# Kernel optimization log

Measured on AMD Instinct MI355X. Metric: run time of the kernel, lower is better.

## Reference

```python
import jax, jax.numpy as jnp
import numpy as np

N_NODES = 100000
N_EDGES = 3200000
D_IN, D_HID, D_OUT = 256, 256, 256
B, V, C = 64, 50, 64
DEC_H1, DEC_H2, N_CLS = 512, 256, 1000
NEG_INF = -1e9


def setup_inputs() -> dict:
    key = jax.random.key(0)
    ks = jax.random.split(key, 20)
    s = lambda d: 1.0 / np.sqrt(d)
    return {
        'edge_index': jax.random.randint(ks[0], (2, N_EDGES), 0, N_NODES, dtype=jnp.int64 if jax.config.jax_enable_x64 else jnp.int32),
        'edge_weight': jax.random.uniform(ks[1], (N_EDGES,), dtype=jnp.float32),
        'codes_x': jax.random.randint(ks[2], (B, V, C), 0, N_NODES, dtype=jnp.int64 if jax.config.jax_enable_x64 else jnp.int32),
        'node_emb': jax.random.normal(ks[3], (N_NODES, D_IN), jnp.float32) * 0.02,
        'W1': jax.random.normal(ks[4], (D_IN, D_HID), jnp.float32) * s(D_IN),
        'b1': jnp.zeros((D_HID,), jnp.float32),
        'W2': jax.random.normal(ks[5], (D_HID, D_OUT), jnp.float32) * s(D_HID),
        'b2': jnp.zeros((D_OUT,), jnp.float32),
        'Wv': jax.random.normal(ks[6], (D_OUT, D_OUT), jnp.float32) * s(D_OUT),
        'uv': jax.random.normal(ks[7], (D_OUT,), jnp.float32) * s(D_OUT),
        'Wp': jax.random.normal(ks[8], (D_OUT, D_OUT), jnp.float32) * s(D_OUT),
        'up': jax.random.normal(ks[9], (D_OUT,), jnp.float32) * s(D_OUT),
        'Wd1': jax.random.normal(ks[10], (D_OUT, DEC_H1), jnp.float32) * s(D_OUT),
        'bd1': jnp.zeros((DEC_H1,), jnp.float32),
        'Wd2': jax.random.normal(ks[11], (DEC_H1, DEC_H2), jnp.float32) * s(DEC_H1),
        'bd2': jnp.zeros((DEC_H2,), jnp.float32),
        'Wd3': jax.random.normal(ks[12], (DEC_H2, N_CLS), jnp.float32) * s(DEC_H2),
        'bd3': jnp.zeros((N_CLS,), jnp.float32),
    }


def reference(edge_index, edge_weight, codes_x, node_emb, W1, b1, W2, b2,
              Wv, uv, Wp, up, Wd1, bd1, Wd2, bd2, Wd3, bd3):
    n = node_emb.shape[0]
    src, dst = edge_index[0], edge_index[1]

    def agg(x):  # weighted message passing: out_i = sum_{e: dst=i} w_e * x[src_e]
        return jax.ops.segment_sum(x[src] * edge_weight[:, None], dst, num_segments=n)

    # 2-layer weighted GCN over the code ontology graph (dropout in eval mode)
    h = jax.nn.relu(agg(node_emb) @ W1 + b1)          # [N, D_hid]
    emb = agg(h) @ W2 + b2                             # [N, D_out]

    # Ragged per-visit code attention, vectorized with masks (code id 0 = padding)
    code_mask = codes_x > 0                            # [B, V, C]
    ce = emb[codes_x]                                  # [B, V, C, D]
    ev = jnp.tanh(jnp.einsum('bvcd,de->bvce', ce, Wv)) @ uv   # [B, V, C]
    av = jax.nn.softmax(jnp.where(code_mask, ev, NEG_INF), axis=-1)
    vemb = jnp.einsum('bvc,bvcd->bvd', av, ce)         # [B, V, D]
    visit_mask = code_mask.any(-1)                     # [B, V]
    vemb = jnp.where(visit_mask[..., None], vemb, 0.0)

    # Per-patient visit attention over valid visits only
    ep = jnp.tanh(vemb @ Wp) @ up                      # [B, V]
    ap = jax.nn.softmax(jnp.where(visit_mask, ep, NEG_INF), axis=-1)
    pemb = jnp.einsum('bv,bvd->bd', ap, vemb)          # [B, D]
    pemb = jnp.where(visit_mask.any(-1)[:, None], pemb, 0.0)  # empty patient -> zeros

    # Decoder MLP classifier (train_type='direct')
    h1 = jax.nn.relu(pemb @ Wd1 + bd1)
    h2 = jax.nn.relu(h1 @ Wd2 + bd2)
    return h2 @ Wd3 + bd3                              # [B, n_classes]
```

## Files before the change

kernel.cpp:

```cpp
#include <hip/hip_runtime.h>
#include <hip/hip_bf16.h>
#include <math.h>


#define D 256
#define BPAT 64
#define VIS 50
#define CODES 64
#define NEG_INF -1e9f
#define MPAD 100096
#define BINB 32
#define NBIN 3125
#define SORTCAP 1536

typedef unsigned short ushort_t;
typedef short short8 __attribute__((ext_vector_type(8)));
typedef float f32x4 __attribute__((ext_vector_type(4)));

__device__ __forceinline__ float blo(unsigned u) { return __uint_as_float(u << 16); }
__device__ __forceinline__ float bhi(unsigned u) { return __uint_as_float(u & 0xffff0000u); }
__device__ __forceinline__ float bf2f(ushort_t u) { return __uint_as_float((unsigned)u << 16); }
__device__ __forceinline__ ushort_t f2bfu(float f) {
    __hip_bfloat16 h = __float2bfloat16(f);
    return *reinterpret_cast<ushort_t*>(&h);
}
__device__ __forceinline__ unsigned pack2(float a, float b) {
    return (unsigned)f2bfu(a) | ((unsigned)f2bfu(b) << 16);
}


__global__ __launch_bounds__(512) void bin_count_kernel(
    const int* __restrict__ ei, int* __restrict__ bincount, int ne) {
    __shared__ int h[NBIN];
    for (int i = threadIdx.x; i < NBIN; i += 512) h[i] = 0;
    __syncthreads();
    int stride = gridDim.x * 512;
    for (int e = blockIdx.x * 512 + threadIdx.x; e < ne; e += stride)
        atomicAdd(&h[ei[(size_t)ne + e] >> 5], 1);
    __syncthreads();
    for (int i = threadIdx.x; i < NBIN; i += 512) {
        int c = h[i];
        if (c) atomicAdd(&bincount[i], c);
    }
}

__global__ __launch_bounds__(64) void bin_scan_kernel(
    const int* __restrict__ bincount, int* __restrict__ binstart,
    int* __restrict__ bincursor, int* __restrict__ rp, int ne, int nn) {
    __shared__ int carry;
    int lane = threadIdx.x;
    if (lane == 0) carry = 0;
    __syncthreads();
    for (int base = 0; base < NBIN; base += 64) {
        int i = base + lane;
        int v = (i < NBIN) ? bincount[i] : 0;
        int x = v;
        #pragma unroll
        for (int d = 1; d < 64; d <<= 1) {
            int y = __shfl_up(x, (unsigned)d, 64);
            if (lane >= d) x += y;
        }
        int c = carry;
        if (i < NBIN) { int ex = c + x - v; binstart[i] = ex; bincursor[i] = ex; }
        __syncthreads();
        if (lane == 63) carry = c + x;
        __syncthreads();
    }
    if (lane == 0) { binstart[NBIN] = ne; rp[nn] = ne; }
}

__global__ __launch_bounds__(512) void partition_kernel(
    const int* __restrict__ ei, const float* __restrict__ ew,
    int* __restrict__ bincursor, uint2* __restrict__ ptmp, int ne) {
    __shared__ int h[NBIN];
    __shared__ int base_[NBIN];
    for (int i = threadIdx.x; i < NBIN; i += 512) h[i] = 0;
    __syncthreads();
    int stride = gridDim.x * 512;
    for (int e = blockIdx.x * 512 + threadIdx.x; e < ne; e += stride)
        atomicAdd(&h[ei[(size_t)ne + e] >> 5], 1);
    __syncthreads();
    for (int i = threadIdx.x; i < NBIN; i += 512) {
        int c = h[i];
        base_[i] = c ? atomicAdd(&bincursor[i], c) : 0;
        h[i] = 0;
    }
    __syncthreads();
    for (int e = blockIdx.x * 512 + threadIdx.x; e < ne; e += stride) {
        int dd = ei[(size_t)ne + e];
        int ss = ei[e];
        float w = ew[e];
        int bin = dd >> 5;
        int r = atomicAdd(&h[bin], 1);
        ptmp[base_[bin] + r] =
            make_uint2((unsigned)ss | ((unsigned)(dd & 31) << 17),
                       __float_as_uint(w));
    }
}

__global__ __launch_bounds__(256) void binsort_kernel(
    const uint2* __restrict__ ptmp, const int* __restrict__ binstart,
    uint2* __restrict__ epair, int* __restrict__ rp) {
    int b = blockIdx.x;
    int tid = threadIdx.x;
    int beg = binstart[b], end = binstart[b + 1];
    int nE = end - beg;
    __shared__ uint2 sbuf[SORTCAP];
    __shared__ int cnt[BINB];
    __shared__ int cur[BINB];
    if (tid < BINB) cnt[tid] = 0;
    __syncthreads();
    if (nE <= SORTCAP) {
        for (int i = tid; i < nE; i += 256) {
            uint2 p = ptmp[beg + i];
            sbuf[i] = p;
            atomicAdd(&cnt[(p.x >> 17) & 31], 1);
        }
        __syncthreads();
        if (tid < BINB) {
            int v = cnt[tid];
            int x = v;
            #pragma unroll
            for (int d = 1; d < BINB; d <<= 1) {
                int y = __shfl_up(x, (unsigned)d, BINB);
                if (tid >= d) x += y;
            }
            int start = beg + x - v;
            cur[tid] = start;
            rp[b * BINB + tid] = start;
        }
        __syncthreads();
        for (int i = tid; i < nE; i += 256) {
            uint2 p = sbuf[i];
            int dl = (p.x >> 17) & 31;
            int pos = atomicAdd(&cur[dl], 1);
            epair[pos] = make_uint2(p.x & 0x1FFFF, p.y);
        }
    } else {
        for (int i = beg + tid; i < end; i += 256)
            atomicAdd(&cnt[(ptmp[i].x >> 17) & 31], 1);
        __syncthreads();
        if (tid < BINB) {
            int v = cnt[tid];
            int x = v;
            #pragma unroll
            for (int d = 1; d < BINB; d <<= 1) {
                int y = __shfl_up(x, (unsigned)d, BINB);
                if (tid >= d) x += y;
            }
            int start = beg + x - v;
            cur[tid] = start;
            rp[b * BINB + tid] = start;
        }
        __syncthreads();
        for (int i = beg + tid; i < end; i += 256) {
            uint2 p = ptmp[i];
            int dl = (p.x >> 17) & 31;
            int pos = atomicAdd(&cur[dl], 1);
            epair[pos] = make_uint2(p.x & 0x1FFFF, p.y);
        }
    }
}

__global__ void cvt_node_kernel(const float* __restrict__ in, ushort_t* __restrict__ out,
                                long n_valid, long n_total) {
    long g = (long)blockIdx.x * blockDim.x + threadIdx.x;
    long ng = n_total >> 2;
    for (long i = g; i < ng; i += (long)gridDim.x * blockDim.x) {
        long e = i << 2;
        uint2 o;
        if (e < n_valid) {
            float4 v = ((const float4*)in)[i];
            o.x = pack2(v.x, v.y);
            o.y = pack2(v.z, v.w);
        } else {
            o.x = 0u; o.y = 0u;
        }
        ((uint2*)out)[i] = o;
    }
}

__global__ __launch_bounds__(256) void transpose_w4_kernel(
    const float* __restrict__ Wa, const float* __restrict__ Wb,
    const float* __restrict__ Wc, const float* __restrict__ Wd,
    ushort_t* __restrict__ Ta, ushort_t* __restrict__ Tb,
    ushort_t* __restrict__ Tc, ushort_t* __restrict__ Td) {
    const float* W;
    ushort_t* Wt;
    switch (blockIdx.z) {
        case 0: W = Wa; Wt = Ta; break;
        case 1: W = Wb; Wt = Tb; break;
        case 2: W = Wc; Wt = Tc; break;
        default: W = Wd; Wt = Td; break;
    }
    __shared__ float t[32][33];
    int bx = blockIdx.x * 32;
    int by = blockIdx.y * 32;
    int lx = threadIdx.x & 31, ly = threadIdx.x >> 5;
    #pragma unroll
    for (int i = 0; i < 32; i += 8)
        t[ly + i][lx] = W[(size_t)(by + ly + i) * 256 + bx + lx];
    __syncthreads();
    #pragma unroll
    for (int i = 0; i < 32; i += 8)
        Wt[(size_t)(bx + ly + i) * 256 + by + lx] = f2bfu(t[lx][ly + i]);
}

__device__ __forceinline__ void acc8(float* a, uint4 v, float w) {
    a[0] += w * blo(v.x); a[1] += w * bhi(v.x);
    a[2] += w * blo(v.y); a[3] += w * bhi(v.y);
    a[4] += w * blo(v.z); a[5] += w * bhi(v.z);
    a[6] += w * blo(v.w); a[7] += w * bhi(v.w);
}

__global__ __launch_bounds__(256) void agg_bf16_kernel(
    const ushort_t* __restrict__ x, const int* __restrict__ rp,
    const uint2* __restrict__ ep, ushort_t* __restrict__ out, int n) {
    int wv = (int)(((size_t)blockIdx.x * blockDim.x + threadIdx.x) >> 6);
    int lane = threadIdx.x & 63;
    if (wv >= n) return;
    int half = lane >> 5;
    int l32 = lane & 31;
    int beg = rp[wv], end = rp[wv + 1];
    float a[8] = {};
    int e = beg;
    for (; e + 16 <= end; e += 16) {
        uint2 p0 = ep[e + half];
        uint2 p1 = ep[e + 2 + half];
        uint2 p2 = ep[e + 4 + half];
        uint2 p3 = ep[e + 6 + half];
        uint2 p4 = ep[e + 8 + half];
        uint2 p5 = ep[e + 10 + half];
        uint2 p6 = ep[e + 12 + half];
        uint2 p7 = ep[e + 14 + half];
        uint4 v0 = ((const uint4*)(x + (size_t)p0.x * D))[l32];
        uint4 v1 = ((const uint4*)(x + (size_t)p1.x * D))[l32];
        uint4 v2 = ((const uint4*)(x + (size_t)p2.x * D))[l32];
        uint4 v3 = ((const uint4*)(x + (size_t)p3.x * D))[l32];
        uint4 v4 = ((const uint4*)(x + (size_t)p4.x * D))[l32];
        uint4 v5 = ((const uint4*)(x + (size_t)p5.x * D))[l32];
        uint4 v6 = ((const uint4*)(x + (size_t)p6.x * D))[l32];
        uint4 v7 = ((const uint4*)(x + (size_t)p7.x * D))[l32];
        acc8(a, v0, __uint_as_float(p0.y));
        acc8(a, v1, __uint_as_float(p1.y));
        acc8(a, v2, __uint_as_float(p2.y));
        acc8(a, v3, __uint_as_float(p3.y));
        acc8(a, v4, __uint_as_float(p4.y));
        acc8(a, v5, __uint_as_float(p5.y));
        acc8(a, v6, __uint_as_float(p6.y));
        acc8(a, v7, __uint_as_float(p7.y));
    }
    for (; e + 4 <= end; e += 4) {
        uint2 p0 = ep[e + half];
        uint2 p1 = ep[e + 2 + half];
        uint4 v0 = ((const uint4*)(x + (size_t)p0.x * D))[l32];
        uint4 v1 = ((const uint4*)(x + (size_t)p1.x * D))[l32];
        acc8(a, v0, __uint_as_float(p0.y));
        acc8(a, v1, __uint_as_float(p1.y));
    }
    for (; e + 2 <= end; e += 2) {
        uint2 p0 = ep[e + half];
        uint4 v0 = ((const uint4*)(x + (size_t)p0.x * D))[l32];
        acc8(a, v0, __uint_as_float(p0.y));
    }
    if (e < end) {
        uint2 p0 = ep[e];
        uint4 v0 = ((const uint4*)(x + (size_t)p0.x * D))[l32];
        acc8(a, v0, half ? 0.f : __uint_as_float(p0.y));
    }
    #pragma unroll
    for (int j = 0; j < 8; ++j) a[j] += __shfl_xor(a[j], 32, 64);
    if (half == 0) {
        uint4 o;
        o.x = pack2(a[0], a[1]); o.y = pack2(a[2], a[3]);
        o.z = pack2(a[4], a[5]); o.w = pack2(a[6], a[7]);
        ((uint4*)(out + (size_t)wv * D))[l32] = o;
    }
}

template<int MODE>
__global__ __launch_bounds__(512) void mfma_gemm_kernel(
    const ushort_t* __restrict__ A, const ushort_t* __restrict__ Wt,
    const float* __restrict__ bias, ushort_t* __restrict__ out,
    const float* __restrict__ u, float* __restrict__ tout, int mvalid) {
    __shared__ __align__(16) ushort_t As[128 * 32];
    __shared__ __align__(16) ushort_t Bs[256 * 32];
    __shared__ float s_t[128];
    const int tid = threadIdx.x;
    const int lane = tid & 63;
    const int wv = tid >> 6;
    const int wr = wv >> 2, wc = wv & 3;
    const size_t brow = (size_t)blockIdx.x * 128;

    const int ra = tid >> 2, ca = tid & 3;
    const int rb1 = ra + 128;
    const int csa = ca ^ ((ra >> 1) & 3);
    const ushort_t* gA  = A  + (brow + ra) * 256 + ca * 8;
    const ushort_t* gB0 = Wt + (size_t)ra  * 256 + ca * 8;
    const ushort_t* gB1 = Wt + (size_t)rb1 * 256 + ca * 8;
    ushort_t* lA  = As + ra * 32 + csa * 8;
    ushort_t* lB0 = Bs + ra * 32 + csa * 8;
    ushort_t* lB1 = Bs + rb1 * 32 + csa * 8;

    const int g = lane >> 4, rl = lane & 15;
    int aoff[4], boff[4];
    #pragma unroll
    for (int m = 0; m < 4; ++m) {
        int row = wr * 64 + m * 16 + rl;
        aoff[m] = row * 32 + (g ^ ((row >> 1) & 3)) * 8;
    }
    #pragma unroll
    for (int n = 0; n < 4; ++n) {
        int row = wc * 64 + n * 16 + rl;
        boff[n] = row * 32 + (g ^ ((row >> 1) & 3)) * 8;
    }

    if (MODE == 2 && tid < 128) s_t[tid] = 0.f;

    f32x4 acc[4][4] = {};
    uint4 va  = *(const uint4*)gA;
    uint4 vb0 = *(const uint4*)gB0;
    uint4 vb1 = *(const uint4*)gB1;

    for (int ks = 0; ks < 8; ++ks) {
        *(uint4*)lA = va; *(uint4*)lB0 = vb0; *(uint4*)lB1 = vb1;
        __syncthreads();
        if (ks < 7) {
            int k0 = (ks + 1) * 32;
            va  = *(const uint4*)(gA + k0);
            vb0 = *(const uint4*)(gB0 + k0);
            vb1 = *(const uint4*)(gB1 + k0);
        }
        short8 af[4], bfv[4];
        #pragma unroll
        for (int m = 0; m < 4; ++m) af[m] = *(const short8*)(As + aoff[m]);
        #pragma unroll
        for (int n = 0; n < 4; ++n) bfv[n] = *(const short8*)(Bs + boff[n]);
        #pragma unroll
        for (int m = 0; m < 4; ++m)
            #pragma unroll
            for (int n = 0; n < 4; ++n)
                acc[m][n] = __builtin_amdgcn_mfma_f32_16x16x32_bf16(
                    af[m], bfv[n], acc[m][n], 0, 0, 0);
        __syncthreads();
    }

    if (MODE == 2) {
        float uvv[4];
        #pragma unroll
        for (int n = 0; n < 4; ++n) uvv[n] = u[wc * 64 + n * 16 + rl];
        #pragma unroll
        for (int m = 0; m < 4; ++m) {
            #pragma unroll
            for (int r = 0; r < 4; ++r) {
                float v = 0.f;
                #pragma unroll
                for (int n = 0; n < 4; ++n) v += tanhf(acc[m][n][r]) * uvv[n];
                v += __shfl_xor(v, 1, 64);
                v += __shfl_xor(v, 2, 64);
                v += __shfl_xor(v, 4, 64);
                v += __shfl_xor(v, 8, 64);
                if (rl == 0) atomicAdd(&s_t[wr * 64 + m * 16 + g * 4 + r], v);
            }
        }
        __syncthreads();
        if (tid < 128 && brow + tid < (size_t)mvalid) tout[brow + tid] = s_t[tid];
    } else {
        #pragma unroll
        for (int m = 0; m < 4; ++m) {
            #pragma unroll
            for (int r = 0; r < 4; ++r) {
                size_t row = brow + wr * 64 + m * 16 + g * 4 + r;
                #pragma unroll
                for (int n = 0; n < 4; ++n) {
                    int col = wc * 64 + n * 16 + rl;
                    float v = acc[m][n][r] + bias[col];
                    if (MODE == 0) v = fmaxf(v, 0.f);
                    out[row * 256 + col] = f2bfu(v);
                }
            }
        }
    }
}

__global__ __launch_bounds__(256) void code_attn_kernel(
    const int* __restrict__ codes, const float* __restrict__ t,
    const ushort_t* __restrict__ emb, ushort_t* __restrict__ vembB,
    int* __restrict__ vmask) {
    int bv = blockIdx.x;
    int tid = threadIdx.x;
    __shared__ int s_codes[CODES];
    __shared__ float s_av[CODES];
    __shared__ int s_valid;
    if (tid < 64) {
        int c = codes[(size_t)bv * CODES + tid];
        s_codes[tid] = c;
        float e = (c > 0) ? t[c] : NEG_INF;
        float m = e;
        #pragma unroll
        for (int d = 32; d; d >>= 1) m = fmaxf(m, __shfl_xor(m, d, 64));
        float ex = expf(e - m);
        float s = ex;
        #pragma unroll
        for (int d = 32; d; d >>= 1) s += __shfl_xor(s, d, 64);
        s_av[tid] = ex / s;
        if (tid == 0) s_valid = (m > -1e8f) ? 1 : 0;
    }
    __syncthreads();
    float acc = 0.f;
    #pragma unroll 4
    for (int c = 0; c < CODES; ++c) {
        int node = s_codes[c];
        if (node > 0) acc += s_av[c] * bf2f(emb[(size_t)node * D + tid]);
    }
    int valid = s_valid;
    vembB[(size_t)bv * D + tid] = f2bfu(valid ? acc : 0.f);
    if (tid == 0) vmask[bv] = valid;
}

__global__ __launch_bounds__(256) void patient_kernel(
    const ushort_t* __restrict__ vembB, const float* __restrict__ epr,
    const int* __restrict__ vmask, float* __restrict__ pemb) {
    int b = blockIdx.x;
    int tid = threadIdx.x;
    __shared__ float s_ap[VIS];
    __shared__ int s_any;
    if (tid < 64) {
        float e = -3e38f;
        if (tid < VIS) e = vmask[b * VIS + tid] ? epr[b * VIS + tid] : NEG_INF;
        float m = e;
        #pragma unroll
        for (int d = 32; d; d >>= 1) m = fmaxf(m, __shfl_xor(m, d, 64));
        float ex = (tid < VIS) ? expf(e - m) : 0.f;
        float s = ex;
        #pragma unroll
        for (int d = 32; d; d >>= 1) s += __shfl_xor(s, d, 64);
        if (tid < VIS) s_ap[tid] = ex / s;
        if (tid == 0) s_any = (m > -1e8f) ? 1 : 0;
    }
    __syncthreads();
    float acc = 0.f;
    for (int v = 0; v < VIS; ++v)
        acc += s_ap[v] * bf2f(vembB[((size_t)b * VIS + v) * D + tid]);
    pemb[b * D + tid] = s_any ? acc : 0.f;
}

__global__ __launch_bounds__(256) void gemm_rowcol(
    const float* __restrict__ A, const float* __restrict__ W,
    const float* __restrict__ bias, float* __restrict__ C,
    int M, int N, int K, int act) {
    int row = blockIdx.x;
    int col = blockIdx.y * 256 + threadIdx.x;
    if (col >= N) return;
    const float* a = A + (size_t)row * K;
    float acc = bias ? bias[col] : 0.f;
    #pragma unroll 4
    for (int k = 0; k < K; ++k) acc = fmaf(a[k], W[(size_t)k * N + col], acc);
    if (act == 1) acc = fmaxf(acc, 0.f);
    C[(size_t)row * N + col] = acc;
}

extern "C" void kernel_launch(void* const* d_in, const int* in_sizes, int n_in,
                              void* d_out, int out_size, void* d_ws, size_t ws_size,
                              hipStream_t stream) {
    const int* edge_index    = (const int*)d_in[0];
    const float* edge_weight = (const float*)d_in[1];
    const int* codes         = (const int*)d_in[2];
    const float* node_emb    = (const float*)d_in[3];
    const float* W1 = (const float*)d_in[4];
    const float* b1 = (const float*)d_in[5];
    const float* W2 = (const float*)d_in[6];
    const float* b2 = (const float*)d_in[7];
    const float* Wv = (const float*)d_in[8];
    const float* uv = (const float*)d_in[9];
    const float* Wp = (const float*)d_in[10];
    const float* up = (const float*)d_in[11];
    const float* Wd1 = (const float*)d_in[12];
    const float* bd1 = (const float*)d_in[13];
    const float* Wd2 = (const float*)d_in[14];
    const float* bd2 = (const float*)d_in[15];
    const float* Wd3 = (const float*)d_in[16];
    const float* bd3 = (const float*)d_in[17];

    const int NE = in_sizes[1];
    const int NN = in_sizes[3] / D;

    char* ws = (char*)d_ws;
    size_t off = 0;
    auto alloc = [&](size_t bytes) -> void* {
        void* p = ws + off;
        off += (bytes + 255) & ~(size_t)255;
        return p;
    };
    ushort_t* nbf  = (ushort_t*)alloc((size_t)MPAD * D * 2);
    ushort_t* aggb = (ushort_t*)alloc((size_t)MPAD * D * 2);
    ushort_t* embB = (ushort_t*)alloc((size_t)MPAD * D * 2);
    uint2* ptmp   = (uint2*)alloc((size_t)NE * 8);
    uint2* epair  = (uint2*)alloc((size_t)NE * 8);
    int* bincount = (int*)alloc((size_t)NBIN * 4);
    int* binstart = (int*)alloc((size_t)(NBIN + 1) * 4);
    int* bincursor= (int*)alloc((size_t)NBIN * 4);
    int* rp       = (int*)alloc((size_t)(NN + 1) * 4);
    ushort_t* W1t = (ushort_t*)alloc(256 * 256 * 2);
    ushort_t* W2t = (ushort_t*)alloc(256 * 256 * 2);
    ushort_t* Wvt = (ushort_t*)alloc(256 * 256 * 2);
    ushort_t* Wpt = (ushort_t*)alloc(256 * 256 * 2);
    float* tbuf  = (float*)alloc((size_t)NN * 4);
    ushort_t* vembB = (ushort_t*)alloc((size_t)BPAT * VIS * D * 2);
    int*   vmask = (int*)  alloc((size_t)BPAT * VIS * 4);
    float* epr   = (float*)alloc((size_t)BPAT * VIS * 4);
    float* pemb  = (float*)alloc((size_t)BPAT * D * 4);
    float* h1    = (float*)alloc((size_t)BPAT * 512 * 4);
    float* h2    = (float*)alloc((size_t)BPAT * D * 4);
    (void)ws_size; (void)n_in; (void)out_size;

    const int ab = NN / 4;

    hipMemsetAsync(bincount, 0, (size_t)NBIN * 4, stream);
    bin_count_kernel<<<256, 512, 0, stream>>>(edge_index, bincount, NE);
    bin_scan_kernel<<<1, 64, 0, stream>>>(bincount, binstart, bincursor, rp, NE, NN);
    partition_kernel<<<128, 512, 0, stream>>>(edge_index, edge_weight,
                                              bincursor, ptmp, NE);
    binsort_kernel<<<NBIN, 256, 0, stream>>>(ptmp, binstart, epair, rp);

    cvt_node_kernel<<<2048, 256, 0, stream>>>(node_emb, nbf, (long)NN * D, (long)MPAD * D);
    transpose_w4_kernel<<<dim3(8, 8, 4), 256, 0, stream>>>(
        W1, W2, Wv, Wp, W1t, W2t, Wvt, Wpt);

    agg_bf16_kernel<<<ab, 256, 0, stream>>>(nbf, rp, epair, aggb, NN);
    mfma_gemm_kernel<0><<<MPAD / 128, 512, 0, stream>>>(
        aggb, W1t, b1, nbf, nullptr, nullptr, 0);

    agg_bf16_kernel<<<ab, 256, 0, stream>>>(nbf, rp, epair, aggb, NN);
    mfma_gemm_kernel<1><<<MPAD / 128, 512, 0, stream>>>(
        aggb, W2t, b2, embB, nullptr, nullptr, 0);

    mfma_gemm_kernel<2><<<MPAD / 128, 512, 0, stream>>>(
        embB, Wvt, nullptr, nullptr, uv, tbuf, NN);

    code_attn_kernel<<<BPAT * VIS, 256, 0, stream>>>(codes, tbuf, embB, vembB, vmask);

    mfma_gemm_kernel<2><<<BPAT * VIS / 128, 512, 0, stream>>>(
        vembB, Wpt, nullptr, nullptr, up, epr, BPAT * VIS);

    patient_kernel<<<BPAT, 256, 0, stream>>>(vembB, epr, vmask, pemb);
    gemm_rowcol<<<dim3(BPAT, 2), 256, 0, stream>>>(pemb, Wd1, bd1, h1, BPAT, 512, D, 1);
    gemm_rowcol<<<dim3(BPAT, 1), 256, 0, stream>>>(h1, Wd2, bd2, h2, BPAT, D, 512, 1);
    gemm_rowcol<<<dim3(BPAT, 4), 256, 0, stream>>>(h2, Wd3, bd3, (float*)d_out, BPAT, 1000, D, 0);
}
```

Measured before the change: 911.1 us.

## Fuse neighbor aggregation with following GEMM via shared-memory staging

Replaces the separate aggregation kernel and MFMA GEMM for each GCN layer with a single kernel. Each block aggregates 64 destination rows into swizzled LDS, then multiplies them by the transposed weight with MFMA and applies bias and activation. This removes the write and re-read of the aggregated intermediate and one launch per layer. In exchange each wave processes 16 rows serially during the gather, so there is less parallelism and latency hiding in the gather phase, and the GEMM tile is smaller.

```diff
diff --git a/kernel.cpp b/kernel.cpp
--- a/kernel.cpp
+++ b/kernel.cpp
@@ -213,68 +213,151 @@
     a[6] += w * blo(v.w); a[7] += w * bhi(v.w);
 }
 
-__global__ __launch_bounds__(256) void agg_bf16_kernel(
+template<int ACT>
+__global__ __launch_bounds__(256) void fused_agg_gemm_kernel(
     const ushort_t* __restrict__ x, const int* __restrict__ rp,
-    const uint2* __restrict__ ep, ushort_t* __restrict__ out, int n) {
-    int wv = (int)(((size_t)blockIdx.x * blockDim.x + threadIdx.x) >> 6);
-    int lane = threadIdx.x & 63;
-    if (wv >= n) return;
-    int half = lane >> 5;
-    int l32 = lane & 31;
-    int beg = rp[wv], end = rp[wv + 1];
-    float a[8] = {};
-    int e = beg;
-    for (; e + 16 <= end; e += 16) {
-        uint2 p0 = ep[e + half];
-        uint2 p1 = ep[e + 2 + half];
-        uint2 p2 = ep[e + 4 + half];
-        uint2 p3 = ep[e + 6 + half];
-        uint2 p4 = ep[e + 8 + half];
-        uint2 p5 = ep[e + 10 + half];
-        uint2 p6 = ep[e + 12 + half];
-        uint2 p7 = ep[e + 14 + half];
-        uint4 v0 = ((const uint4*)(x + (size_t)p0.x * D))[l32];
-        uint4 v1 = ((const uint4*)(x + (size_t)p1.x * D))[l32];
-        uint4 v2 = ((const uint4*)(x + (size_t)p2.x * D))[l32];
-        uint4 v3 = ((const uint4*)(x + (size_t)p3.x * D))[l32];
-        uint4 v4 = ((const uint4*)(x + (size_t)p4.x * D))[l32];
-        uint4 v5 = ((const uint4*)(x + (size_t)p5.x * D))[l32];
-        uint4 v6 = ((const uint4*)(x + (size_t)p6.x * D))[l32];
-        uint4 v7 = ((const uint4*)(x + (size_t)p7.x * D))[l32];
-        acc8(a, v0, __uint_as_float(p0.y));
-        acc8(a, v1, __uint_as_float(p1.y));
-        acc8(a, v2, __uint_as_float(p2.y));
-        acc8(a, v3, __uint_as_float(p3.y));
-        acc8(a, v4, __uint_as_float(p4.y));
-        acc8(a, v5, __uint_as_float(p5.y));
-        acc8(a, v6, __uint_as_float(p6.y));
-        acc8(a, v7, __uint_as_float(p7.y));
-    }
-    for (; e + 4 <= end; e += 4) {
-        uint2 p0 = ep[e + half];
-        uint2 p1 = ep[e + 2 + half];
-        uint4 v0 = ((const uint4*)(x + (size_t)p0.x * D))[l32];
-        uint4 v1 = ((const uint4*)(x + (size_t)p1.x * D))[l32];
-        acc8(a, v0, __uint_as_float(p0.y));
-        acc8(a, v1, __uint_as_float(p1.y));
-    }
-    for (; e + 2 <= end; e += 2) {
-        uint2 p0 = ep[e + half];
-        uint4 v0 = ((const uint4*)(x + (size_t)p0.x * D))[l32];
-        acc8(a, v0, __uint_as_float(p0.y));
-    }
-    if (e < end) {
-        uint2 p0 = ep[e];
-        uint4 v0 = ((const uint4*)(x + (size_t)p0.x * D))[l32];
-        acc8(a, v0, half ? 0.f : __uint_as_float(p0.y));
-    }
+    const uint2* __restrict__ ep, const ushort_t* __restrict__ Wt,
+    const float* __restrict__ bias, ushort_t* __restrict__ out, int nn) {
+    __shared__ __align__(16) ushort_t As[8 * 64 * 32];
+    __shared__ __align__(16) ushort_t Bs[256 * 32];
+    const int tid = threadIdx.x;
+    const int lane = tid & 63;
+    const int wid = tid >> 6;
+    const int half = lane >> 5;
+    const int l32 = lane & 31;
+    const int brow = blockIdx.x * 64;
+
+    const int brQ = tid >> 2, bgQ = tid & 3;
+    const ushort_t* gB0 = Wt + (size_t)brQ * 256 + bgQ * 8;
+    uint4 bpre0 = *(const uint4*)(gB0);
+    uint4 bpre1 = *(const uint4*)(gB0 + 64 * 256);
+    uint4 bpre2 = *(const uint4*)(gB0 + 128 * 256);
+    uint4 bpre3 = *(const uint4*)(gB0 + 192 * 256);
+
+    for (int r16 = 0; r16 < 16; ++r16) {
+        int row = wid * 16 + r16;
+        int dst = brow + row;
+        float a[8] = {};
+        if (dst < nn) {
+            int beg = rp[dst], end = rp[dst + 1];
+            int e = beg;
+            for (; e + 16 <= end; e += 16) {
+                uint2 p0 = ep[e + half];
+                uint2 p1 = ep[e + 2 + half];
+                uint2 p2 = ep[e + 4 + half];
+                uint2 p3 = ep[e + 6 + half];
+                uint2 p4 = ep[e + 8 + half];
+                uint2 p5 = ep[e + 10 + half];
+                uint2 p6 = ep[e + 12 + half];
+                uint2 p7 = ep[e + 14 + half];
+                uint4 v0 = ((const uint4*)(x + (size_t)p0.x * D))[l32];
+                uint4 v1 = ((const uint4*)(x + (size_t)p1.x * D))[l32];
+                uint4 v2 = ((const uint4*)(x + (size_t)p2.x * D))[l32];
+                uint4 v3 = ((const uint4*)(x + (size_t)p3.x * D))[l32];
+                uint4 v4 = ((const uint4*)(x + (size_t)p4.x * D))[l32];
+                uint4 v5 = ((const uint4*)(x + (size_t)p5.x * D))[l32];
+                uint4 v6 = ((const uint4*)(x + (size_t)p6.x * D))[l32];
+                uint4 v7 = ((const uint4*)(x + (size_t)p7.x * D))[l32];
+                acc8(a, v0, __uint_as_float(p0.y));
+                acc8(a, v1, __uint_as_float(p1.y));
+                acc8(a, v2, __uint_as_float(p2.y));
+                acc8(a, v3, __uint_as_float(p3.y));
+                acc8(a, v4, __uint_as_float(p4.y));
+                acc8(a, v5, __uint_as_float(p5.y));
+                acc8(a, v6, __uint_as_float(p6.y));
+                acc8(a, v7, __uint_as_float(p7.y));
+            }
+            for (; e + 4 <= end; e += 4) {
+                uint2 p0 = ep[e + half];
+                uint2 p1 = ep[e + 2 + half];
+                uint4 v0 = ((const uint4*)(x + (size_t)p0.x * D))[l32];
+                uint4 v1 = ((const uint4*)(x + (size_t)p1.x * D))[l32];
+                acc8(a, v0, __uint_as_float(p0.y));
+                acc8(a, v1, __uint_as_float(p1.y));
+            }
+            for (; e + 2 <= end; e += 2) {
+                uint2 p0 = ep[e + half];
+                uint4 v0 = ((const uint4*)(x + (size_t)p0.x * D))[l32];
+                acc8(a, v0, __uint_as_float(p0.y));
+            }
+            if (e < end) {
+                uint2 p0 = ep[e];
+                uint4 v0 = ((const uint4*)(x + (size_t)p0.x * D))[l32];
+                acc8(a, v0, half ? 0.f : __uint_as_float(p0.y));
+            }
+        }
+        #pragma unroll
+        for (int j = 0; j < 8; ++j) a[j] += __shfl_xor(a[j], 32, 64);
+        if (half == 0) {
+            uint4 o;
+            o.x = pack2(a[0], a[1]); o.y = pack2(a[2], a[3]);
+            o.z = pack2(a[4], a[5]); o.w = pack2(a[6], a[7]);
+            int kc  = l32 >> 2;
+            int grp = (l32 & 3) ^ ((row >> 1) & 3);
+            ((uint4*)As)[(kc * 64 + row) * 4 + grp] = o;
+        }
+    }
+    __syncthreads();
+
+    const int g = lane >> 4, rl = lane & 15;
+    int bw0 = (brQ +   0) * 4 + (bgQ ^ ((brQ >> 1) & 3));
+    int bw1 = (brQ +  64) * 4 + (bgQ ^ (((brQ + 64) >> 1) & 3));
+    int bw2 = (brQ + 128) * 4 + (bgQ ^ (((brQ + 128) >> 1) & 3));
+    int bw3 = (brQ + 192) * 4 + (bgQ ^ (((brQ + 192) >> 1) & 3));
+    int aoff[4], boff[4];
     #pragma unroll
-    for (int j = 0; j < 8; ++j) a[j] += __shfl_xor(a[j], 32, 64);
-    if (half == 0) {
-        uint4 o;
-        o.x = pack2(a[0], a[1]); o.y = pack2(a[2], a[3]);
-        o.z = pack2(a[4], a[5]); o.w = pack2(a[6], a[7]);
-        ((uint4*)(out + (size_t)wv * D))[l32] = o;
+    for (int m = 0; m < 4; ++m) {
+        int row = m * 16 + rl;
+        aoff[m] = row * 4 + (g ^ ((row >> 1) & 3));
+    }
+    #pragma unroll
+    for (int n = 0; n < 4; ++n) {
+        int col = wid * 64 + n * 16 + rl;
+        boff[n] = col * 4 + (g ^ ((col >> 1) & 3));
+    }
+
+    f32x4 acc[4][4] = {};
+    for (int kc = 0; kc < 8; ++kc) {
+        ((uint4*)Bs)[bw0] = bpre0;
+        ((uint4*)Bs)[bw1] = bpre1;
+        ((uint4*)Bs)[bw2] = bpre2;
+        ((uint4*)Bs)[bw3] = bpre3;
+        __syncthreads();
+        if (kc < 7) {
+            int k0 = (kc + 1) * 32;
+            bpre0 = *(const uint4*)(gB0 + k0);
+            bpre1 = *(const uint4*)(gB0 + 64 * 256 + k0);
+            bpre2 = *(const uint4*)(gB0 + 128 * 256 + k0);
+            bpre3 = *(const uint4*)(gB0 + 192 * 256 + k0);
+        }
+        const ushort_t* Ac = As + kc * 64 * 32;
+        short8 af[4], bfv[4];
+        #pragma unroll
+        for (int m = 0; m < 4; ++m) af[m] = *(const short8*)(Ac + aoff[m] * 8);
+        #pragma unroll
+        for (int n = 0; n < 4; ++n) bfv[n] = *(const short8*)(Bs + boff[n] * 8);
+        #pragma unroll
+        for (int m = 0; m < 4; ++m)
+            #pragma unroll
+            for (int n = 0; n < 4; ++n)
+                acc[m][n] = __builtin_amdgcn_mfma_f32_16x16x32_bf16(
+                    af[m], bfv[n], acc[m][n], 0, 0, 0);
+        __syncthreads();
+    }
+
+    #pragma unroll
+    for (int m = 0; m < 4; ++m) {
+        #pragma unroll
+        for (int r = 0; r < 4; ++r) {
+            size_t row = (size_t)brow + m * 16 + g * 4 + r;
+            #pragma unroll
+            for (int n = 0; n < 4; ++n) {
+                int col = wid * 64 + n * 16 + rl;
+                float v = acc[m][n][r] + bias[col];
+                if (ACT == 1) v = fmaxf(v, 0.f);
+                out[row * 256 + col] = f2bfu(v);
+            }
+        }
     }
 }
 
@@ -493,7 +576,7 @@
         return p;
     };
     ushort_t* nbf  = (ushort_t*)alloc((size_t)MPAD * D * 2);
-    ushort_t* aggb = (ushort_t*)alloc((size_t)MPAD * D * 2);
+    ushort_t* hbuf = (ushort_t*)alloc((size_t)MPAD * D * 2);
     ushort_t* embB = (ushort_t*)alloc((size_t)MPAD * D * 2);
     uint2* ptmp   = (uint2*)alloc((size_t)NE * 8);
     uint2* epair  = (uint2*)alloc((size_t)NE * 8);
@@ -514,8 +597,6 @@
     float* h2    = (float*)alloc((size_t)BPAT * D * 4);
     (void)ws_size; (void)n_in; (void)out_size;
 
-    const int ab = NN / 4;
-
     hipMemsetAsync(bincount, 0, (size_t)NBIN * 4, stream);
     bin_count_kernel<<<256, 512, 0, stream>>>(edge_index, bincount, NE);
     bin_scan_kernel<<<1, 64, 0, stream>>>(bincount, binstart, bincursor, rp, NE, NN);
@@ -527,13 +608,11 @@
     transpose_w4_kernel<<<dim3(8, 8, 4), 256, 0, stream>>>(
         W1, W2, Wv, Wp, W1t, W2t, Wvt, Wpt);
 
-    agg_bf16_kernel<<<ab, 256, 0, stream>>>(nbf, rp, epair, aggb, NN);
-    mfma_gemm_kernel<0><<<MPAD / 128, 512, 0, stream>>>(
-        aggb, W1t, b1, nbf, nullptr, nullptr, 0);
-
-    agg_bf16_kernel<<<ab, 256, 0, stream>>>(nbf, rp, epair, aggb, NN);
-    mfma_gemm_kernel<1><<<MPAD / 128, 512, 0, stream>>>(
-        aggb, W2t, b2, embB, nullptr, nullptr, 0);
+    fused_agg_gemm_kernel<1><<<MPAD / 64, 256, 0, stream>>>(
+        nbf, rp, epair, W1t, b1, hbuf, NN);
+
+    fused_agg_gemm_kernel<0><<<MPAD / 64, 256, 0, stream>>>(
+        hbuf, rp, epair, W2t, b2, embB, NN);
 
     mfma_gemm_kernel<2><<<MPAD / 128, 512, 0, stream>>>(
         embB, Wvt, nullptr, nullptr, uv, tbuf, NN);
```

After: 993.6 us. 9.1% more time.

## Reorder GCN to transform-then-aggregate and fuse fp32 conversion into first GEMM

Applied to the files above, without the earlier changes.

Uses linearity of aggregation to compute agg(X)W as agg(XW), so each layer runs the GEMM first and then aggregates, with bias and ReLU fused into the aggregation epilogue. A new GEMM reads fp32 node embeddings directly and converts them to bf16 while staging into LDS, which removes the separate conversion kernel and its extra pass over memory. Rounding happens at different points, so numerics shift slightly. Padded rows of the intermediate buffers may hold garbage instead of zeros.

```diff
diff --git a/kernel.cpp b/kernel.cpp
--- a/kernel.cpp
+++ b/kernel.cpp
@@ -159,24 +159,6 @@
             int pos = atomicAdd(&cur[dl], 1);
             epair[pos] = make_uint2(p.x & 0x1FFFF, p.y);
         }
-    }
-}
-
-__global__ void cvt_node_kernel(const float* __restrict__ in, ushort_t* __restrict__ out,
-                                long n_valid, long n_total) {
-    long g = (long)blockIdx.x * blockDim.x + threadIdx.x;
-    long ng = n_total >> 2;
-    for (long i = g; i < ng; i += (long)gridDim.x * blockDim.x) {
-        long e = i << 2;
-        uint2 o;
-        if (e < n_valid) {
-            float4 v = ((const float4*)in)[i];
-            o.x = pack2(v.x, v.y);
-            o.y = pack2(v.z, v.w);
-        } else {
-            o.x = 0u; o.y = 0u;
-        }
-        ((uint2*)out)[i] = o;
     }
 }
 
@@ -213,9 +195,11 @@
     a[6] += w * blo(v.w); a[7] += w * bhi(v.w);
 }
 
+template<int ACT>
 __global__ __launch_bounds__(256) void agg_bf16_kernel(
     const ushort_t* __restrict__ x, const int* __restrict__ rp,
-    const uint2* __restrict__ ep, ushort_t* __restrict__ out, int n) {
+    const uint2* __restrict__ ep, const float* __restrict__ bias,
+    ushort_t* __restrict__ out, int n) {
     int wv = (int)(((size_t)blockIdx.x * blockDim.x + threadIdx.x) >> 6);
     int lane = threadIdx.x & 63;
     if (wv >= n) return;
@@ -271,10 +255,103 @@
     #pragma unroll
     for (int j = 0; j < 8; ++j) a[j] += __shfl_xor(a[j], 32, 64);
     if (half == 0) {
+        float4 b0 = ((const float4*)bias)[l32 * 2];
+        float4 b1 = ((const float4*)bias)[l32 * 2 + 1];
+        a[0] += b0.x; a[1] += b0.y; a[2] += b0.z; a[3] += b0.w;
+        a[4] += b1.x; a[5] += b1.y; a[6] += b1.z; a[7] += b1.w;
+        if (ACT == 1) {
+            #pragma unroll
+            for (int j = 0; j < 8; ++j) a[j] = fmaxf(a[j], 0.f);
+        }
         uint4 o;
         o.x = pack2(a[0], a[1]); o.y = pack2(a[2], a[3]);
         o.z = pack2(a[4], a[5]); o.w = pack2(a[6], a[7]);
         ((uint4*)(out + (size_t)wv * D))[l32] = o;
+    }
+}
+
+__global__ __launch_bounds__(512) void gemm_f32a_kernel(
+    const float* __restrict__ Af, const ushort_t* __restrict__ Wt,
+    ushort_t* __restrict__ out, int nvalid) {
+    __shared__ __align__(16) ushort_t As[128 * 32];
+    __shared__ __align__(16) ushort_t Bs[256 * 32];
+    const int tid = threadIdx.x;
+    const int lane = tid & 63;
+    const int wv = tid >> 6;
+    const int wr = wv >> 2, wc = wv & 3;
+    const size_t brow = (size_t)blockIdx.x * 128;
+
+    const int ra = tid >> 2, ca = tid & 3;
+    const int rb1 = ra + 128;
+    const int csa = ca ^ ((ra >> 1) & 3);
+    const int arow = (int)brow + ra;
+    const bool aval = arow < nvalid;
+    const float* gAf = Af + (size_t)arow * 256 + ca * 8;
+    const ushort_t* gB0 = Wt + (size_t)ra  * 256 + ca * 8;
+    const ushort_t* gB1 = Wt + (size_t)rb1 * 256 + ca * 8;
+    ushort_t* lA  = As + ra * 32 + csa * 8;
+    ushort_t* lB0 = Bs + ra * 32 + csa * 8;
+    ushort_t* lB1 = Bs + rb1 * 32 + csa * 8;
+
+    const int g = lane >> 4, rl = lane & 15;
+    int aoff[4], boff[4];
+    #pragma unroll
+    for (int m = 0; m < 4; ++m) {
+        int row = wr * 64 + m * 16 + rl;
+        aoff[m] = row * 32 + (g ^ ((row >> 1) & 3)) * 8;
+    }
+    #pragma unroll
+    for (int n = 0; n < 4; ++n) {
+        int row = wc * 64 + n * 16 + rl;
+        boff[n] = row * 32 + (g ^ ((row >> 1) & 3)) * 8;
+    }
+
+    f32x4 acc[4][4] = {};
+    float4 pa0 = make_float4(0.f, 0.f, 0.f, 0.f), pa1 = pa0;
+    if (aval) { pa0 = *(const float4*)gAf; pa1 = *(const float4*)(gAf + 4); }
+    uint4 vb0 = *(const uint4*)gB0;
+    uint4 vb1 = *(const uint4*)gB1;
+
+    for (int ks = 0; ks < 8; ++ks) {
+        uint4 va;
+        va.x = pack2(pa0.x, pa0.y); va.y = pack2(pa0.z, pa0.w);
+        va.z = pack2(pa1.x, pa1.y); va.w = pack2(pa1.z, pa1.w);
+        *(uint4*)lA = va; *(uint4*)lB0 = vb0; *(uint4*)lB1 = vb1;
+        __syncthreads();
+        if (ks < 7) {
+            int k0 = (ks + 1) * 32;
+            if (aval) {
+                pa0 = *(const float4*)(gAf + k0);
+                pa1 = *(const float4*)(gAf + k0 + 4);
+            }
+            vb0 = *(const uint4*)(gB0 + k0);
+            vb1 = *(const uint4*)(gB1 + k0);
+        }
+        short8 af[4], bfv[4];
+        #pragma unroll
+        for (int m = 0; m < 4; ++m) af[m] = *(const short8*)(As + aoff[m]);
+        #pragma unroll
+        for (int n = 0; n < 4; ++n) bfv[n] = *(const short8*)(Bs + boff[n]);
+        #pragma unroll
+        for (int m = 0; m < 4; ++m)
+            #pragma unroll
+            for (int n = 0; n < 4; ++n)
+                acc[m][n] = __builtin_amdgcn_mfma_f32_16x16x32_bf16(
+                    af[m], bfv[n], acc[m][n], 0, 0, 0);
+        __syncthreads();
+    }
+
+    #pragma unroll
+    for (int m = 0; m < 4; ++m) {
+        #pragma unroll
+        for (int r = 0; r < 4; ++r) {
+            size_t row = brow + wr * 64 + m * 16 + g * 4 + r;
+            #pragma unroll
+            for (int n = 0; n < 4; ++n) {
+                int col = wc * 64 + n * 16 + rl;
+                out[row * 256 + col] = f2bfu(acc[m][n][r]);
+            }
+        }
     }
 }
 
@@ -374,8 +451,7 @@
                 #pragma unroll
                 for (int n = 0; n < 4; ++n) {
                     int col = wc * 64 + n * 16 + rl;
-                    float v = acc[m][n][r] + bias[col];
-                    if (MODE == 0) v = fmaxf(v, 0.f);
+                    float v = acc[m][n][r] + (bias ? bias[col] : 0.f);
                     out[row * 256 + col] = f2bfu(v);
                 }
             }
@@ -492,8 +568,8 @@
         off += (bytes + 255) & ~(size_t)255;
         return p;
     };
-    ushort_t* nbf  = (ushort_t*)alloc((size_t)MPAD * D * 2);
-    ushort_t* aggb = (ushort_t*)alloc((size_t)MPAD * D * 2);
+    ushort_t* zbuf = (ushort_t*)alloc((size_t)MPAD * D * 2);
+    ushort_t* hbuf = (ushort_t*)alloc((size_t)MPAD * D * 2);
     ushort_t* embB = (ushort_t*)alloc((size_t)MPAD * D * 2);
     uint2* ptmp   = (uint2*)alloc((size_t)NE * 8);
     uint2* epair  = (uint2*)alloc((size_t)NE * 8);
@@ -523,17 +599,15 @@
                                               bincursor, ptmp, NE);
     binsort_kernel<<<NBIN, 256, 0, stream>>>(ptmp, binstart, epair, rp);
 
-    cvt_node_kernel<<<2048, 256, 0, stream>>>(node_emb, nbf, (long)NN * D, (long)MPAD * D);
     transpose_w4_kernel<<<dim3(8, 8, 4), 256, 0, stream>>>(
         W1, W2, Wv, Wp, W1t, W2t, Wvt, Wpt);
 
-    agg_bf16_kernel<<<ab, 256, 0, stream>>>(nbf, rp, epair, aggb, NN);
-    mfma_gemm_kernel<0><<<MPAD / 128, 512, 0, stream>>>(
-        aggb, W1t, b1, nbf, nullptr, nullptr, 0);
-
-    agg_bf16_kernel<<<ab, 256, 0, stream>>>(nbf, rp, epair, aggb, NN);
+    gemm_f32a_kernel<<<MPAD / 128, 512, 0, stream>>>(node_emb, W1t, zbuf, NN);
+    agg_bf16_kernel<1><<<ab, 256, 0, stream>>>(zbuf, rp, epair, b1, hbuf, NN);
+
     mfma_gemm_kernel<1><<<MPAD / 128, 512, 0, stream>>>(
-        aggb, W2t, b2, embB, nullptr, nullptr, 0);
+        hbuf, W2t, nullptr, zbuf, nullptr, nullptr, 0);
+    agg_bf16_kernel<0><<<ab, 256, 0, stream>>>(zbuf, rp, epair, b2, embB, NN);
 
     mfma_gemm_kernel<2><<<MPAD / 128, 512, 0, stream>>>(
         embB, Wvt, nullptr, nullptr, uv, tbuf, NN);
```

Result: no change. 893.9 us (-1.9%).
